# Performance work log

Hardware: AMD Instinct MI355X
Metric: run time of the kernel (lower is better)

Reference implementation:

```python
import jax, jax.numpy as jnp
import numpy as np

D_MODEL = 768
N_HEADS = 12
HEAD = 64
B, T = 2, 2048


def setup_inputs() -> dict:
    key = jax.random.key(0)
    k1, k2, k3 = jax.random.split(key, 3)
    x = jax.random.normal(k1, (B, T, D_MODEL), dtype=jnp.float32)
    W1 = jax.random.normal(k2, (3 * D_MODEL, D_MODEL), dtype=jnp.float32) * (1.0 / np.sqrt(D_MODEL))
    b1 = jnp.zeros((3 * D_MODEL,), dtype=jnp.float32)
    W2 = jax.random.normal(k3, (D_MODEL, D_MODEL), dtype=jnp.float32) * (1.0 / np.sqrt(D_MODEL))
    b2 = jnp.zeros((D_MODEL,), dtype=jnp.float32)
    return {"x": x, "W1": W1, "b1": b1, "W2": W2, "b2": b2}


def reference(x, W1, b1, W2, b2):
    Bx, Tx, C = x.shape
    qkv = jnp.einsum('btc,fc->btf', x, W1) + b1            # (B,T,3C)
    q, k, v = jnp.split(qkv, 3, axis=-1)
    # (B,T,H,Dh) -> (B,H,T,Dh)
    q = q.reshape(Bx, Tx, N_HEADS, HEAD).transpose(0, 2, 1, 3)
    k = k.reshape(Bx, Tx, N_HEADS, HEAD).transpose(0, 2, 1, 3)
    v = v.reshape(Bx, Tx, N_HEADS, HEAD).transpose(0, 2, 1, 3)
    scale = 1.0 / np.sqrt(HEAD)
    scores = jnp.einsum('bhqd,bhkd->bhqk', q, k) * scale   # (B,H,T,T)
    causal = jnp.tril(jnp.ones((Tx, Tx), dtype=bool))
    scores = jnp.where(causal, scores, jnp.finfo(scores.dtype).min)
    attn = jax.nn.softmax(scores, axis=-1)
    o = jnp.einsum('bhqk,bhkd->bhqd', attn, v)             # (B,H,T,Dh)
    o = o.transpose(0, 2, 1, 3).reshape(Bx, Tx, C)
    return jnp.einsum('btc,fc->btf', o, W2) + b2
```

## Files before the change

### kernel.cpp

```cpp
#include <hip/hip_runtime.h>


typedef float f32x4 __attribute__((ext_vector_type(4)));
typedef __bf16 bf16x8 __attribute__((ext_vector_type(8)));
typedef unsigned int u32x4 __attribute__((ext_vector_type(4)));

#define D_MODEL 768
#define F3 2304
#define NHEADS 12
#define HEAD 64
#define BB 2
#define TT 2048
#define MROWS (BB*TT)
#define KDIM 768
#define LOG2E 1.44269504f
#define NX (MROWS*D_MODEL)
#define NW1 (F3*KDIM)
#define NW2 (D_MODEL*KDIM)

__device__ __forceinline__ unsigned short f2bf(float f) {
    unsigned int u = __float_as_uint(f);
    u += 0x7fffu + ((u >> 16) & 1u);
    return (unsigned short)(u >> 16);
}
__device__ __forceinline__ unsigned int pack2bf(float a, float b) {
    unsigned int ua = __float_as_uint(a), ub = __float_as_uint(b);
    ua += 0x7fffu + ((ua >> 16) & 1u);
    ub += 0x7fffu + ((ub >> 16) & 1u);
    return (ua >> 16) | (ub & 0xffff0000u);
}

__device__ __forceinline__ void async_copy16(unsigned short* lds, const unsigned short* g) {
    __builtin_amdgcn_global_load_lds(
        (const __attribute__((address_space(1))) unsigned int*)(const void*)g,
        (__attribute__((address_space(3))) unsigned int*)(void*)lds,
        16, 0, 0);
}

__global__ void prep(const float* __restrict__ x, const float* __restrict__ W1,
                     const float* __restrict__ W2, unsigned short* __restrict__ xb,
                     unsigned short* __restrict__ w1b, unsigned short* __restrict__ w2b) {
    const int i4 = (blockIdx.x * blockDim.x + threadIdx.x) * 4;
    const float* src; unsigned short* dst; int off;
    if (i4 < NX)                  { src = x;  dst = xb;  off = i4; }
    else if (i4 < NX + NW1)       { src = W1; dst = w1b; off = i4 - NX; }
    else if (i4 < NX + NW1 + NW2) { src = W2; dst = w2b; off = i4 - NX - NW1; }
    else return;
    float4 v = *(const float4*)(src + off);
    uint2 o;
    o.x = pack2bf(v.x, v.y);
    o.y = pack2bf(v.z, v.w);
    *(uint2*)(dst + off) = o;
}

__global__ __launch_bounds__(256, 4) void gemm1(
    const unsigned short* __restrict__ A, const unsigned short* __restrict__ Bw,
    const float* __restrict__ bias, int K,
    unsigned short* __restrict__ Qb, unsigned short* __restrict__ Kb,
    unsigned short* __restrict__ VT)
{
    __shared__ unsigned short As[128*64];
    __shared__ unsigned short Bs[96*64];
    const int tid  = threadIdx.x;
    const int wave = tid >> 6;
    const int lane = tid & 63;
    const int quad = lane >> 4;
    const int l16  = lane & 15;

    const int F   = blockIdx.x;
    const int xcd = F & 7;
    const int idx = F >> 3;
    const int bm  = (xcd & 3) * 8 + (idx & 7);
    const int bn  = (xcd >> 2) * 12 + (idx >> 3);
    const int m0  = bm * 128;
    const int n0  = bn * 96;
    const int seg = bn >> 3;

    const int wm = (wave >> 1) * 64;
    const int wn = (wave & 1) * 48;

    f32x4 acc[4][3] = {};

    const unsigned short* Ablk = A + (size_t)m0 * K;
    const unsigned short* Bblk = Bw + (size_t)n0 * K;
    const int srow = tid >> 3;
    const int scol = ((tid & 7) ^ (srow & 7)) * 8;

    for (int k0 = 0; k0 < K; k0 += 64) {
        #pragma unroll
        for (int r = 0; r < 4; ++r)
            async_copy16(As + r*2048 + tid*8,
                         Ablk + (size_t)(r*32 + srow) * K + k0 + scol);
        #pragma unroll
        for (int r = 0; r < 3; ++r)
            async_copy16(Bs + r*2048 + tid*8,
                         Bblk + (size_t)(r*32 + srow) * K + k0 + scol);
        asm volatile("s_waitcnt vmcnt(0)" ::: "memory");
        __syncthreads();

        #pragma unroll
        for (int kc2 = 0; kc2 < 2; ++kc2) {
            const int pos = ((kc2*4 + quad) ^ (l16 & 7)) * 8;
            bf16x8 a[4], b[3];
            #pragma unroll
            for (int i = 0; i < 4; ++i)
                a[i] = *(const bf16x8*)(As + (wm + i*16 + l16)*64 + pos);
            #pragma unroll
            for (int j = 0; j < 3; ++j)
                b[j] = *(const bf16x8*)(Bs + (wn + j*16 + l16)*64 + pos);
            #pragma unroll
            for (int i = 0; i < 4; ++i)
                #pragma unroll
                for (int j = 0; j < 3; ++j)
                    acc[i][j] = __builtin_amdgcn_mfma_f32_16x16x32_bf16(a[i], b[j], acc[i][j], 0, 0, 0);
        }
        __syncthreads();
    }

    if (seg < 2) {
        #pragma unroll
        for (int j = 0; j < 3; ++j) {
            const int n = n0 + wn + j*16 + l16;
            const float bv = bias[n];
            const int f = n - seg * 768;
            const int h = f >> 6, d = f & 63;
            #pragma unroll
            for (int i = 0; i < 4; ++i)
                #pragma unroll
                for (int r = 0; r < 4; ++r) {
                    const int m = m0 + wm + i*16 + quad*4 + r;
                    const int b = m >> 11, t = m & 2047;
                    const size_t idxq = (((size_t)(b*NHEADS + h)) * TT + t) * HEAD + d;
                    const float v = acc[i][j][r] + bv;
                    if (seg == 0) Qb[idxq] = f2bf(v * (0.125f * LOG2E));
                    else          Kb[idxq] = f2bf(v);
                }
        }
    } else {
        #pragma unroll
        for (int j = 0; j < 3; ++j) {
            const int n = n0 + wn + j*16 + l16;
            const float bv = bias[n];
            const int f = n - 1536;
            const int h = f >> 6, d = f & 63;
            #pragma unroll
            for (int i = 0; i < 4; ++i) {
                const int m = m0 + wm + i*16 + quad*4;
                const int b = m >> 11, t = m & 2047;
                uint2 pk;
                pk.x = pack2bf(acc[i][j][0] + bv, acc[i][j][1] + bv);
                pk.y = pack2bf(acc[i][j][2] + bv, acc[i][j][3] + bv);
                *(uint2*)(VT + ((size_t)(b*NHEADS + h) * HEAD + d) * TT + t) = pk;
            }
        }
    }
}

__global__ __launch_bounds__(256, 4) void gemm2(
    const unsigned short* __restrict__ A, const unsigned short* __restrict__ Bw,
    const float* __restrict__ bias, int K, float* __restrict__ Cout)
{
    __shared__ unsigned short As[64*64];
    __shared__ unsigned short Bs[96*64];
    const int tid  = threadIdx.x;
    const int wave = tid >> 6;
    const int lane = tid & 63;
    const int quad = lane >> 4;
    const int l16  = lane & 15;

    const int F   = blockIdx.x;
    const int xcd = F & 7;
    const int idx = F >> 3;
    const int m0  = ((xcd & 3) * 16 + (idx & 15)) * 64;
    const int n0  = ((xcd >> 2) * 4 + (idx >> 4)) * 96;

    const int wm = (wave >> 1) * 32;
    const int wn = (wave & 1) * 48;

    f32x4 acc[2][3] = {};

    const unsigned short* Ablk = A + (size_t)m0 * K;
    const unsigned short* Bblk = Bw + (size_t)n0 * K;
    const int srow = tid >> 3;
    const int scol = ((tid & 7) ^ (srow & 7)) * 8;

    for (int k0 = 0; k0 < K; k0 += 64) {
        #pragma unroll
        for (int r = 0; r < 2; ++r)
            async_copy16(As + r*2048 + tid*8,
                         Ablk + (size_t)(r*32 + srow) * K + k0 + scol);
        #pragma unroll
        for (int r = 0; r < 3; ++r)
            async_copy16(Bs + r*2048 + tid*8,
                         Bblk + (size_t)(r*32 + srow) * K + k0 + scol);
        asm volatile("s_waitcnt vmcnt(0)" ::: "memory");
        __syncthreads();

        #pragma unroll
        for (int kc2 = 0; kc2 < 2; ++kc2) {
            const int pos = ((kc2*4 + quad) ^ (l16 & 7)) * 8;
            bf16x8 a[2], b[3];
            #pragma unroll
            for (int i = 0; i < 2; ++i)
                a[i] = *(const bf16x8*)(As + (wm + i*16 + l16)*64 + pos);
            #pragma unroll
            for (int j = 0; j < 3; ++j)
                b[j] = *(const bf16x8*)(Bs + (wn + j*16 + l16)*64 + pos);
            #pragma unroll
            for (int i = 0; i < 2; ++i)
                #pragma unroll
                for (int j = 0; j < 3; ++j)
                    acc[i][j] = __builtin_amdgcn_mfma_f32_16x16x32_bf16(a[i], b[j], acc[i][j], 0, 0, 0);
        }
        __syncthreads();
    }

    #pragma unroll
    for (int j = 0; j < 3; ++j) {
        const int n = n0 + wn + j*16 + l16;
        const float bv = bias[n];
        #pragma unroll
        for (int i = 0; i < 2; ++i)
            #pragma unroll
            for (int r = 0; r < 4; ++r) {
                const int m = m0 + wm + i*16 + quad*4 + r;
                Cout[(size_t)m * D_MODEL + n] = acc[i][j][r] + bv;
            }
    }
}

__global__ __launch_bounds__(256, 3) void attn(
    const unsigned short* __restrict__ Qb, const unsigned short* __restrict__ Kb,
    const unsigned short* __restrict__ VT, unsigned short* __restrict__ Ob)
{
    __shared__ unsigned short Ks[128*64];
    __shared__ unsigned short Vt[64*128];

    const int tid  = threadIdx.x;
    const int wave = tid >> 6;
    const int lane = tid & 63;
    const int quad = lane >> 4;
    const int l16  = lane & 15;

    const int F    = blockIdx.y * 32 + blockIdx.x;
    const int xcd  = F & 7;
    const int slot = F >> 3;
    const int bh   = xcd * 3 + (slot >> 5);
    const int j    = slot & 31;
    const size_t hbase = (size_t)bh * TT * HEAD;

    const int krow = tid >> 3;
    const int kchunk = ((tid & 7) ^ (krow & 7)) * 8;
    const int vrow = tid >> 4;
    const int vchunk = ((tid & 15) ^ vrow) * 8;

    #pragma unroll 1
    for (int seg = 0; seg < 2; ++seg) {
        const int t   = seg ? (63 - j) : j;
        const int nkt = (t >> 2) + 1;
        const int q0  = t * 32;

        bf16x8 qreg[2][2];
        #pragma unroll
        for (int qs = 0; qs < 2; ++qs) {
            const unsigned short* qp = Qb + hbase + (size_t)(q0 + qs*16 + l16) * HEAD + quad*8;
            qreg[qs][0] = *(const bf16x8*)(qp);
            qreg[qs][1] = *(const bf16x8*)(qp + 32);
        }

        f32x4 oacc[2][4] = {};
        float lst[2] = {0.f, 0.f};

        for (int kt = 0; kt < nkt; ++kt) {
            __syncthreads();

            const unsigned short* ksrc = Kb + hbase + (size_t)kt * 128 * HEAD;
            #pragma unroll
            for (int ii = 0; ii < 4; ++ii)
                async_copy16(Ks + ii*2048 + tid*8,
                             ksrc + (size_t)(ii*32 + krow) * 64 + kchunk);
            #pragma unroll
            for (int ii = 0; ii < 4; ++ii)
                async_copy16(Vt + ii*2048 + tid*8,
                             VT + hbase + (size_t)(ii*16 + vrow) * TT + kt*128 + vchunk);
            asm volatile("s_waitcnt vmcnt(0)" ::: "memory");
            __syncthreads();

            f32x4 s[2][2] = {};
            #pragma unroll
            for (int kc2 = 0; kc2 < 2; ++kc2) {
                const int pos = ((kc2*4 + quad) ^ (l16 & 7)) * 8;
                #pragma unroll
                for (int n = 0; n < 2; ++n) {
                    const bf16x8 ak = *(const bf16x8*)(Ks + (wave*32 + n*16 + l16)*64 + pos);
                    #pragma unroll
                    for (int qs = 0; qs < 2; ++qs)
                        s[n][qs] = __builtin_amdgcn_mfma_f32_16x16x32_bf16(ak, qreg[qs][kc2], s[n][qs], 0, 0, 0);
                }
            }

            if (kt == (t >> 2)) {
                const int kq = kt*128 + wave*32 + quad*4;
                #pragma unroll
                for (int n = 0; n < 2; ++n)
                    #pragma unroll
                    for (int qs = 0; qs < 2; ++qs)
                        #pragma unroll
                        for (int r = 0; r < 4; ++r)
                            if (kq + n*16 + r > q0 + qs*16 + l16) s[n][qs][r] = -1e30f;
            }

            uint2 pck[2][2];
            #pragma unroll
            for (int n = 0; n < 2; ++n)
                #pragma unroll
                for (int qs = 0; qs < 2; ++qs) {
                    const float p0 = exp2f(s[n][qs][0]);
                    const float p1 = exp2f(s[n][qs][1]);
                    const float p2 = exp2f(s[n][qs][2]);
                    const float p3 = exp2f(s[n][qs][3]);
                    lst[qs] += (p0 + p1) + (p2 + p3);
                    pck[n][qs].x = pack2bf(p0, p1);
                    pck[n][qs].y = pack2bf(p2, p3);
                }

            bf16x8 ap[2];
            #pragma unroll
            for (int qs = 0; qs < 2; ++qs) {
                u32x4 pw = {pck[0][qs].x, pck[0][qs].y, pck[1][qs].x, pck[1][qs].y};
                ap[qs] = __builtin_bit_cast(bf16x8, pw);
            }
            const int g1 = wave*4 + (quad >> 1);
            #pragma unroll
            for (int dt = 0; dt < 4; ++dt) {
                const unsigned short* vr = Vt + (dt*16 + l16)*128;
                const int c1 = ((g1     ^ l16) * 8) + (quad & 1) * 4;
                const int c2 = (((g1+2) ^ l16) * 8) + (quad & 1) * 4;
                const uint2 lo = *(const uint2*)(vr + c1);
                const uint2 hi = *(const uint2*)(vr + c2);
                u32x4 vv = {lo.x, lo.y, hi.x, hi.y};
                const bf16x8 bv = __builtin_bit_cast(bf16x8, vv);
                #pragma unroll
                for (int qs = 0; qs < 2; ++qs)
                    oacc[qs][dt] = __builtin_amdgcn_mfma_f32_16x16x32_bf16(ap[qs], bv, oacc[qs][dt], 0, 0, 0);
            }
        }

        #pragma unroll
        for (int qs = 0; qs < 2; ++qs) {
            lst[qs] += __shfl_xor(lst[qs], 16);
            lst[qs] += __shfl_xor(lst[qs], 32);
        }

        __syncthreads();
        {
            float* O1 = (float*)Ks;
            float* O2 = (float*)Ks + 2048;
            float* O3 = (float*)Vt;
            float* Lb = (float*)Vt + 2048;
            if (wave != 0) {
                float* ob = (wave == 1) ? O1 : (wave == 2) ? O2 : O3;
                #pragma unroll
                for (int qs = 0; qs < 2; ++qs)
                    #pragma unroll
                    for (int dt = 0; dt < 4; ++dt)
                        #pragma unroll
                        for (int r = 0; r < 4; ++r)
                            ob[(qs*16 + quad*4 + r)*64 + dt*16 + l16] = oacc[qs][dt][r];
                if (lane < 16) {
                    Lb[(wave-1)*32 + l16]      = lst[0];
                    Lb[(wave-1)*32 + 16 + l16] = lst[1];
                }
            }
            __syncthreads();
            if (wave == 0) {
                float linv[2], lr[2][4];
                #pragma unroll
                for (int qs = 0; qs < 2; ++qs) {
                    const float lt = lst[qs] + Lb[qs*16 + l16] + Lb[32 + qs*16 + l16]
                                             + Lb[64 + qs*16 + l16];
                    linv[qs] = 1.0f / lt;
                }
                #pragma unroll
                for (int qs = 0; qs < 2; ++qs)
                    #pragma unroll
                    for (int r = 0; r < 4; ++r)
                        lr[qs][r] = __shfl(linv[qs], quad*4 + r);
                const int b = bh / NHEADS, h = bh % NHEADS;
                #pragma unroll
                for (int qs = 0; qs < 2; ++qs)
                    #pragma unroll
                    for (int r = 0; r < 4; ++r) {
                        const int m = b * TT + q0 + qs*16 + quad*4 + r;
                        unsigned short* dst = Ob + (size_t)m * D_MODEL + h*HEAD;
                        #pragma unroll
                        for (int dt = 0; dt < 4; ++dt) {
                            const int idx = (qs*16 + quad*4 + r)*64 + dt*16 + l16;
                            const float v = oacc[qs][dt][r] + O1[idx] + O2[idx] + O3[idx];
                            dst[dt*16 + l16] = f2bf(v * lr[qs][r]);
                        }
                    }
            }
        }
    }
}

extern "C" void kernel_launch(void* const* d_in, const int* in_sizes, int n_in,
                              void* d_out, int out_size, void* d_ws, size_t ws_size,
                              hipStream_t stream) {
    const float* x  = (const float*)d_in[0];
    const float* W1 = (const float*)d_in[1];
    const float* b1 = (const float*)d_in[2];
    const float* W2 = (const float*)d_in[3];
    const float* b2 = (const float*)d_in[4];
    float* out = (float*)d_out;

    unsigned short* ws = (unsigned short*)d_ws;
    unsigned short* xb  = ws;
    unsigned short* w1b = xb  + (size_t)NX;
    unsigned short* w2b = w1b + (size_t)NW1;
    unsigned short* Qb  = w2b + (size_t)NW2;
    unsigned short* Kb  = Qb + (size_t)BB*NHEADS*TT*HEAD;
    unsigned short* VT  = Kb + (size_t)BB*NHEADS*TT*HEAD;
    unsigned short* Ob  = VT + (size_t)BB*NHEADS*TT*HEAD;

    prep<<<((NX + NW1 + NW2)/4 + 255)/256, 256, 0, stream>>>(
        x, W1, W2, xb, w1b, w2b);

    gemm1<<<768, 256, 0, stream>>>(
        xb, w1b, b1, KDIM, Qb, Kb, VT);

    attn<<<dim3(32, BB*NHEADS), 256, 0, stream>>>(Qb, Kb, VT, Ob);

    gemm2<<<512, 256, 0, stream>>>(
        Ob, w2b, b2, KDIM, out);
}
```

Baseline: 146.6 us.

## Double-buffer GEMM shared-memory tiles to overlap global loads with MFMA

Both projection GEMMs now split K into 32-wide steps with two LDS buffers, issuing the async copy for the next step before computing the current one. The aim is to hide global-load latency that the old single-buffer load-wait-compute loop exposed. The cost is twice as many barriers and waits per unit of K, plus a new XOR swizzle for the 32-wide rows. Each step also has less MFMA work (one k-chunk instead of two), which may leave too little compute to cover the load.

```diff
diff --git a/kernel.cpp b/kernel.cpp
--- a/kernel.cpp
+++ b/kernel.cpp
@@ -59,8 +59,8 @@
     unsigned short* __restrict__ Qb, unsigned short* __restrict__ Kb,
     unsigned short* __restrict__ VT)
 {
-    __shared__ unsigned short As[128*64];
-    __shared__ unsigned short Bs[96*64];
+    __shared__ unsigned short As[2][128*32];
+    __shared__ unsigned short Bs[2][96*32];
     const int tid  = threadIdx.x;
     const int wave = tid >> 6;
     const int lane = tid & 63;
@@ -83,39 +83,51 @@
 
     const unsigned short* Ablk = A + (size_t)m0 * K;
     const unsigned short* Bblk = Bw + (size_t)n0 * K;
-    const int srow = tid >> 3;
-    const int scol = ((tid & 7) ^ (srow & 7)) * 8;
-
-    for (int k0 = 0; k0 < K; k0 += 64) {
-        #pragma unroll
-        for (int r = 0; r < 4; ++r)
-            async_copy16(As + r*2048 + tid*8,
-                         Ablk + (size_t)(r*32 + srow) * K + k0 + scol);
-        #pragma unroll
-        for (int r = 0; r < 3; ++r)
-            async_copy16(Bs + r*2048 + tid*8,
-                         Bblk + (size_t)(r*32 + srow) * K + k0 + scol);
+
+    const int ra0 = tid >> 2,         ca0 = (tid & 3) ^ ((ra0 >> 1) & 3);
+    const int ra1 = (tid + 256) >> 2, ca1 = (tid & 3) ^ ((ra1 >> 1) & 3);
+    const int rb1 = (tid + 256) >> 2, cb1 = (tid & 3) ^ ((rb1 >> 1) & 3);
+
+    #define G1_STAGE(buf, k0)                                                   \
+        do {                                                                    \
+            async_copy16(&As[buf][tid*8],       Ablk + (size_t)ra0*K + (k0) + ca0*8); \
+            async_copy16(&As[buf][2048 + tid*8],Ablk + (size_t)ra1*K + (k0) + ca1*8); \
+            async_copy16(&Bs[buf][tid*8],       Bblk + (size_t)ra0*K + (k0) + ca0*8); \
+            if (tid < 128)                                                      \
+                async_copy16(&Bs[buf][2048 + tid*8], Bblk + (size_t)rb1*K + (k0) + cb1*8); \
+        } while (0)
+
+    G1_STAGE(0, 0);
+    asm volatile("s_waitcnt vmcnt(0)" ::: "memory");
+    __syncthreads();
+
+    for (int t = 0; t < 24; ++t) {
+        const int cur = t & 1;
+        if (t < 23) G1_STAGE(cur ^ 1, (t + 1) * 32);
+
+        const unsigned short* Ab = As[cur];
+        const unsigned short* Bb = Bs[cur];
+        bf16x8 a[4], b[3];
+        #pragma unroll
+        for (int i = 0; i < 4; ++i) {
+            const int row = wm + i*16 + l16;
+            a[i] = *(const bf16x8*)(Ab + row*32 + ((quad ^ ((row >> 1) & 3)) * 8));
+        }
+        #pragma unroll
+        for (int j = 0; j < 3; ++j) {
+            const int row = wn + j*16 + l16;
+            b[j] = *(const bf16x8*)(Bb + row*32 + ((quad ^ ((row >> 1) & 3)) * 8));
+        }
+        #pragma unroll
+        for (int i = 0; i < 4; ++i)
+            #pragma unroll
+            for (int j = 0; j < 3; ++j)
+                acc[i][j] = __builtin_amdgcn_mfma_f32_16x16x32_bf16(a[i], b[j], acc[i][j], 0, 0, 0);
+
         asm volatile("s_waitcnt vmcnt(0)" ::: "memory");
         __syncthreads();
-
-        #pragma unroll
-        for (int kc2 = 0; kc2 < 2; ++kc2) {
-            const int pos = ((kc2*4 + quad) ^ (l16 & 7)) * 8;
-            bf16x8 a[4], b[3];
-            #pragma unroll
-            for (int i = 0; i < 4; ++i)
-                a[i] = *(const bf16x8*)(As + (wm + i*16 + l16)*64 + pos);
-            #pragma unroll
-            for (int j = 0; j < 3; ++j)
-                b[j] = *(const bf16x8*)(Bs + (wn + j*16 + l16)*64 + pos);
-            #pragma unroll
-            for (int i = 0; i < 4; ++i)
-                #pragma unroll
-                for (int j = 0; j < 3; ++j)
-                    acc[i][j] = __builtin_amdgcn_mfma_f32_16x16x32_bf16(a[i], b[j], acc[i][j], 0, 0, 0);
-        }
-        __syncthreads();
     }
+    #undef G1_STAGE
 
     if (seg < 2) {
         #pragma unroll
@@ -160,8 +172,8 @@
     const unsigned short* __restrict__ A, const unsigned short* __restrict__ Bw,
     const float* __restrict__ bias, int K, float* __restrict__ Cout)
 {
-    __shared__ unsigned short As[64*64];
-    __shared__ unsigned short Bs[96*64];
+    __shared__ unsigned short As[2][64*32];
+    __shared__ unsigned short Bs[2][96*32];
     const int tid  = threadIdx.x;
     const int wave = tid >> 6;
     const int lane = tid & 63;
@@ -181,39 +193,49 @@
 
     const unsigned short* Ablk = A + (size_t)m0 * K;
     const unsigned short* Bblk = Bw + (size_t)n0 * K;
-    const int srow = tid >> 3;
-    const int scol = ((tid & 7) ^ (srow & 7)) * 8;
-
-    for (int k0 = 0; k0 < K; k0 += 64) {
-        #pragma unroll
-        for (int r = 0; r < 2; ++r)
-            async_copy16(As + r*2048 + tid*8,
-                         Ablk + (size_t)(r*32 + srow) * K + k0 + scol);
-        #pragma unroll
-        for (int r = 0; r < 3; ++r)
-            async_copy16(Bs + r*2048 + tid*8,
-                         Bblk + (size_t)(r*32 + srow) * K + k0 + scol);
+
+    const int ra0 = tid >> 2,         ca0 = (tid & 3) ^ ((ra0 >> 1) & 3);
+    const int rb1 = (tid + 256) >> 2, cb1 = (tid & 3) ^ ((rb1 >> 1) & 3);
+
+    #define G2_STAGE(buf, k0)                                                   \
+        do {                                                                    \
+            async_copy16(&As[buf][tid*8],  Ablk + (size_t)ra0*K + (k0) + ca0*8); \
+            async_copy16(&Bs[buf][tid*8],  Bblk + (size_t)ra0*K + (k0) + ca0*8); \
+            if (tid < 128)                                                      \
+                async_copy16(&Bs[buf][2048 + tid*8], Bblk + (size_t)rb1*K + (k0) + cb1*8); \
+        } while (0)
+
+    G2_STAGE(0, 0);
+    asm volatile("s_waitcnt vmcnt(0)" ::: "memory");
+    __syncthreads();
+
+    for (int t = 0; t < 24; ++t) {
+        const int cur = t & 1;
+        if (t < 23) G2_STAGE(cur ^ 1, (t + 1) * 32);
+
+        const unsigned short* Ab = As[cur];
+        const unsigned short* Bb = Bs[cur];
+        bf16x8 a[2], b[3];
+        #pragma unroll
+        for (int i = 0; i < 2; ++i) {
+            const int row = wm + i*16 + l16;
+            a[i] = *(const bf16x8*)(Ab + row*32 + ((quad ^ ((row >> 1) & 3)) * 8));
+        }
+        #pragma unroll
+        for (int j = 0; j < 3; ++j) {
+            const int row = wn + j*16 + l16;
+            b[j] = *(const bf16x8*)(Bb + row*32 + ((quad ^ ((row >> 1) & 3)) * 8));
+        }
+        #pragma unroll
+        for (int i = 0; i < 2; ++i)
+            #pragma unroll
+            for (int j = 0; j < 3; ++j)
+                acc[i][j] = __builtin_amdgcn_mfma_f32_16x16x32_bf16(a[i], b[j], acc[i][j], 0, 0, 0);
+
         asm volatile("s_waitcnt vmcnt(0)" ::: "memory");
         __syncthreads();
-
-        #pragma unroll
-        for (int kc2 = 0; kc2 < 2; ++kc2) {
-            const int pos = ((kc2*4 + quad) ^ (l16 & 7)) * 8;
-            bf16x8 a[2], b[3];
-            #pragma unroll
-            for (int i = 0; i < 2; ++i)
-                a[i] = *(const bf16x8*)(As + (wm + i*16 + l16)*64 + pos);
-            #pragma unroll
-            for (int j = 0; j < 3; ++j)
-                b[j] = *(const bf16x8*)(Bs + (wn + j*16 + l16)*64 + pos);
-            #pragma unroll
-            for (int i = 0; i < 2; ++i)
-                #pragma unroll
-                for (int j = 0; j < 3; ++j)
-                    acc[i][j] = __builtin_amdgcn_mfma_f32_16x16x32_bf16(a[i], b[j], acc[i][j], 0, 0, 0);
-        }
-        __syncthreads();
     }
+    #undef G2_STAGE
 
     #pragma unroll
     for (int j = 0; j < 3; ++j) {
```

After: 150.2 us. +2.5%, slower.

## Share K/V tile loads between paired low and high query blocks in attention

Applied to the files above, without the earlier changes.

Each block used to process its two causal query tiles (j and 63-j) one after the other, loading K/V tiles into shared memory separately for each. The new code runs a single key-tile loop over the longer range and applies each loaded K/V tile to both query tiles, so the shorter tile's K/V loads and LDS fragment reads are no longer repeated. This roughly halves global-to-LDS traffic and synchronisation for the attention stage. The cost is higher register pressure from two sets of Q registers and accumulators, which may lower occupancy.

```diff
diff --git a/kernel.cpp b/kernel.cpp
--- a/kernel.cpp
+++ b/kernel.cpp
@@ -249,160 +249,182 @@
     const int j    = slot & 31;
     const size_t hbase = (size_t)bh * TT * HEAD;
 
+    const int nktl = (j >> 2) + 1;
+    const int nkth = 17 - nktl;
+    const int q0l  = j * 32;
+    const int q0h  = (63 - j) * 32;
+
     const int krow = tid >> 3;
     const int kchunk = ((tid & 7) ^ (krow & 7)) * 8;
     const int vrow = tid >> 4;
     const int vchunk = ((tid & 15) ^ vrow) * 8;
 
-    #pragma unroll 1
-    for (int seg = 0; seg < 2; ++seg) {
-        const int t   = seg ? (63 - j) : j;
-        const int nkt = (t >> 2) + 1;
-        const int q0  = t * 32;
-
-        bf16x8 qreg[2][2];
-        #pragma unroll
-        for (int qs = 0; qs < 2; ++qs) {
-            const unsigned short* qp = Qb + hbase + (size_t)(q0 + qs*16 + l16) * HEAD + quad*8;
-            qreg[qs][0] = *(const bf16x8*)(qp);
-            qreg[qs][1] = *(const bf16x8*)(qp + 32);
-        }
-
-        f32x4 oacc[2][4] = {};
-        float lst[2] = {0.f, 0.f};
-
-        for (int kt = 0; kt < nkt; ++kt) {
-            __syncthreads();
-
-            const unsigned short* ksrc = Kb + hbase + (size_t)kt * 128 * HEAD;
-            #pragma unroll
-            for (int ii = 0; ii < 4; ++ii)
-                async_copy16(Ks + ii*2048 + tid*8,
-                             ksrc + (size_t)(ii*32 + krow) * 64 + kchunk);
-            #pragma unroll
-            for (int ii = 0; ii < 4; ++ii)
-                async_copy16(Vt + ii*2048 + tid*8,
-                             VT + hbase + (size_t)(ii*16 + vrow) * TT + kt*128 + vchunk);
-            asm volatile("s_waitcnt vmcnt(0)" ::: "memory");
-            __syncthreads();
-
-            f32x4 s[2][2] = {};
-            #pragma unroll
-            for (int kc2 = 0; kc2 < 2; ++kc2) {
-                const int pos = ((kc2*4 + quad) ^ (l16 & 7)) * 8;
-                #pragma unroll
-                for (int n = 0; n < 2; ++n) {
-                    const bf16x8 ak = *(const bf16x8*)(Ks + (wave*32 + n*16 + l16)*64 + pos);
-                    #pragma unroll
-                    for (int qs = 0; qs < 2; ++qs)
-                        s[n][qs] = __builtin_amdgcn_mfma_f32_16x16x32_bf16(ak, qreg[qs][kc2], s[n][qs], 0, 0, 0);
-                }
-            }
-
-            if (kt == (t >> 2)) {
-                const int kq = kt*128 + wave*32 + quad*4;
-                #pragma unroll
-                for (int n = 0; n < 2; ++n)
-                    #pragma unroll
-                    for (int qs = 0; qs < 2; ++qs)
-                        #pragma unroll
-                        for (int r = 0; r < 4; ++r)
-                            if (kq + n*16 + r > q0 + qs*16 + l16) s[n][qs][r] = -1e30f;
-            }
-
-            uint2 pck[2][2];
+    bf16x8 qregl[2][2], qregh[2][2];
+    #pragma unroll
+    for (int qs = 0; qs < 2; ++qs) {
+        const unsigned short* ql = Qb + hbase + (size_t)(q0l + qs*16 + l16) * HEAD + quad*8;
+        const unsigned short* qh = Qb + hbase + (size_t)(q0h + qs*16 + l16) * HEAD + quad*8;
+        qregl[qs][0] = *(const bf16x8*)(ql);
+        qregl[qs][1] = *(const bf16x8*)(ql + 32);
+        qregh[qs][0] = *(const bf16x8*)(qh);
+        qregh[qs][1] = *(const bf16x8*)(qh + 32);
+    }
+
+    f32x4 oaccl[2][4] = {}, oacch[2][4] = {};
+    float lstl[2] = {0.f, 0.f}, lsth[2] = {0.f, 0.f};
+
+    const int g1 = wave*4 + (quad >> 1);
+
+    #define TILE_COMPUTE(QREG, OACC, LST, Q0, DOMASK, KT)                       \
+    do {                                                                        \
+        f32x4 s[2][2] = {};                                                     \
+        _Pragma("unroll")                                                       \
+        for (int kc2 = 0; kc2 < 2; ++kc2)                                       \
+            _Pragma("unroll")                                                   \
+            for (int n = 0; n < 2; ++n)                                         \
+                _Pragma("unroll")                                               \
+                for (int qs = 0; qs < 2; ++qs)                                  \
+                    s[n][qs] = __builtin_amdgcn_mfma_f32_16x16x32_bf16(         \
+                        ak[kc2][n], QREG[qs][kc2], s[n][qs], 0, 0, 0);          \
+        if (DOMASK) {                                                           \
+            const int kq = (KT)*128 + wave*32 + quad*4;                         \
+            _Pragma("unroll")                                                   \
+            for (int n = 0; n < 2; ++n)                                         \
+                _Pragma("unroll")                                               \
+                for (int qs = 0; qs < 2; ++qs)                                  \
+                    _Pragma("unroll")                                           \
+                    for (int r = 0; r < 4; ++r)                                 \
+                        if (kq + n*16 + r > (Q0) + qs*16 + l16)                 \
+                            s[n][qs][r] = -1e30f;                               \
+        }                                                                       \
+        uint2 pck[2][2];                                                        \
+        _Pragma("unroll")                                                       \
+        for (int n = 0; n < 2; ++n)                                             \
+            _Pragma("unroll")                                                   \
+            for (int qs = 0; qs < 2; ++qs) {                                    \
+                const float p0 = exp2f(s[n][qs][0]);                            \
+                const float p1 = exp2f(s[n][qs][1]);                            \
+                const float p2 = exp2f(s[n][qs][2]);                            \
+                const float p3 = exp2f(s[n][qs][3]);                            \
+                LST[qs] += (p0 + p1) + (p2 + p3);                               \
+                pck[n][qs].x = pack2bf(p0, p1);                                 \
+                pck[n][qs].y = pack2bf(p2, p3);                                 \
+            }                                                                   \
+        _Pragma("unroll")                                                       \
+        for (int qs = 0; qs < 2; ++qs) {                                        \
+            u32x4 pw = {pck[0][qs].x, pck[0][qs].y, pck[1][qs].x, pck[1][qs].y};\
+            const bf16x8 ap = __builtin_bit_cast(bf16x8, pw);                   \
+            _Pragma("unroll")                                                   \
+            for (int dt = 0; dt < 4; ++dt)                                      \
+                OACC[qs][dt] = __builtin_amdgcn_mfma_f32_16x16x32_bf16(         \
+                    ap, bv[dt], OACC[qs][dt], 0, 0, 0);                         \
+        }                                                                       \
+    } while (0)
+
+    for (int kt = 0; kt < nkth; ++kt) {
+        __syncthreads();
+
+        const unsigned short* ksrc = Kb + hbase + (size_t)kt * 128 * HEAD;
+        #pragma unroll
+        for (int ii = 0; ii < 4; ++ii)
+            async_copy16(Ks + ii*2048 + tid*8,
+                         ksrc + (size_t)(ii*32 + krow) * 64 + kchunk);
+        #pragma unroll
+        for (int ii = 0; ii < 4; ++ii)
+            async_copy16(Vt + ii*2048 + tid*8,
+                         VT + hbase + (size_t)(ii*16 + vrow) * TT + kt*128 + vchunk);
+        asm volatile("s_waitcnt vmcnt(0)" ::: "memory");
+        __syncthreads();
+
+        bf16x8 ak[2][2];
+        #pragma unroll
+        for (int kc2 = 0; kc2 < 2; ++kc2) {
+            const int pos = ((kc2*4 + quad) ^ (l16 & 7)) * 8;
             #pragma unroll
             for (int n = 0; n < 2; ++n)
-                #pragma unroll
-                for (int qs = 0; qs < 2; ++qs) {
-                    const float p0 = exp2f(s[n][qs][0]);
-                    const float p1 = exp2f(s[n][qs][1]);
-                    const float p2 = exp2f(s[n][qs][2]);
-                    const float p3 = exp2f(s[n][qs][3]);
-                    lst[qs] += (p0 + p1) + (p2 + p3);
-                    pck[n][qs].x = pack2bf(p0, p1);
-                    pck[n][qs].y = pack2bf(p2, p3);
-                }
-
-            bf16x8 ap[2];
-            #pragma unroll
-            for (int qs = 0; qs < 2; ++qs) {
-                u32x4 pw = {pck[0][qs].x, pck[0][qs].y, pck[1][qs].x, pck[1][qs].y};
-                ap[qs] = __builtin_bit_cast(bf16x8, pw);
-            }
-            const int g1 = wave*4 + (quad >> 1);
-            #pragma unroll
-            for (int dt = 0; dt < 4; ++dt) {
-                const unsigned short* vr = Vt + (dt*16 + l16)*128;
-                const int c1 = ((g1     ^ l16) * 8) + (quad & 1) * 4;
-                const int c2 = (((g1+2) ^ l16) * 8) + (quad & 1) * 4;
-                const uint2 lo = *(const uint2*)(vr + c1);
-                const uint2 hi = *(const uint2*)(vr + c2);
-                u32x4 vv = {lo.x, lo.y, hi.x, hi.y};
-                const bf16x8 bv = __builtin_bit_cast(bf16x8, vv);
-                #pragma unroll
-                for (int qs = 0; qs < 2; ++qs)
-                    oacc[qs][dt] = __builtin_amdgcn_mfma_f32_16x16x32_bf16(ap[qs], bv, oacc[qs][dt], 0, 0, 0);
-            }
-        }
-
-        #pragma unroll
-        for (int qs = 0; qs < 2; ++qs) {
-            lst[qs] += __shfl_xor(lst[qs], 16);
-            lst[qs] += __shfl_xor(lst[qs], 32);
-        }
-
-        __syncthreads();
-        {
-            float* O1 = (float*)Ks;
-            float* O2 = (float*)Ks + 2048;
-            float* O3 = (float*)Vt;
-            float* Lb = (float*)Vt + 2048;
-            if (wave != 0) {
-                float* ob = (wave == 1) ? O1 : (wave == 2) ? O2 : O3;
-                #pragma unroll
-                for (int qs = 0; qs < 2; ++qs)
-                    #pragma unroll
-                    for (int dt = 0; dt < 4; ++dt)
-                        #pragma unroll
-                        for (int r = 0; r < 4; ++r)
-                            ob[(qs*16 + quad*4 + r)*64 + dt*16 + l16] = oacc[qs][dt][r];
-                if (lane < 16) {
-                    Lb[(wave-1)*32 + l16]      = lst[0];
-                    Lb[(wave-1)*32 + 16 + l16] = lst[1];
-                }
-            }
-            __syncthreads();
-            if (wave == 0) {
-                float linv[2], lr[2][4];
-                #pragma unroll
-                for (int qs = 0; qs < 2; ++qs) {
-                    const float lt = lst[qs] + Lb[qs*16 + l16] + Lb[32 + qs*16 + l16]
-                                             + Lb[64 + qs*16 + l16];
-                    linv[qs] = 1.0f / lt;
-                }
-                #pragma unroll
-                for (int qs = 0; qs < 2; ++qs)
-                    #pragma unroll
-                    for (int r = 0; r < 4; ++r)
-                        lr[qs][r] = __shfl(linv[qs], quad*4 + r);
-                const int b = bh / NHEADS, h = bh % NHEADS;
-                #pragma unroll
-                for (int qs = 0; qs < 2; ++qs)
-                    #pragma unroll
-                    for (int r = 0; r < 4; ++r) {
-                        const int m = b * TT + q0 + qs*16 + quad*4 + r;
-                        unsigned short* dst = Ob + (size_t)m * D_MODEL + h*HEAD;
-                        #pragma unroll
-                        for (int dt = 0; dt < 4; ++dt) {
-                            const int idx = (qs*16 + quad*4 + r)*64 + dt*16 + l16;
-                            const float v = oacc[qs][dt][r] + O1[idx] + O2[idx] + O3[idx];
-                            dst[dt*16 + l16] = f2bf(v * lr[qs][r]);
-                        }
-                    }
-            }
-        }
-    }
+                ak[kc2][n] = *(const bf16x8*)(Ks + (wave*32 + n*16 + l16)*64 + pos);
+        }
+        bf16x8 bv[4];
+        #pragma unroll
+        for (int dt = 0; dt < 4; ++dt) {
+            const unsigned short* vr = Vt + (dt*16 + l16)*128;
+            const int c1 = ((g1     ^ l16) * 8) + (quad & 1) * 4;
+            const int c2 = (((g1+2) ^ l16) * 8) + (quad & 1) * 4;
+            const uint2 lo = *(const uint2*)(vr + c1);
+            const uint2 hi = *(const uint2*)(vr + c2);
+            u32x4 vv = {lo.x, lo.y, hi.x, hi.y};
+            bv[dt] = __builtin_bit_cast(bf16x8, vv);
+        }
+
+        TILE_COMPUTE(qregh, oacch, lsth, q0h, (kt == nkth - 1), kt);
+        if (kt < nktl)
+            TILE_COMPUTE(qregl, oaccl, lstl, q0l, (kt == nktl - 1), kt);
+    }
+    #undef TILE_COMPUTE
+
+    #pragma unroll
+    for (int qs = 0; qs < 2; ++qs) {
+        lstl[qs] += __shfl_xor(lstl[qs], 16);
+        lstl[qs] += __shfl_xor(lstl[qs], 32);
+        lsth[qs] += __shfl_xor(lsth[qs], 16);
+        lsth[qs] += __shfl_xor(lsth[qs], 32);
+    }
+
+    #define COMBINE(OACC, LST, Q0)                                              \
+    do {                                                                        \
+        float* O1 = (float*)Ks;                                                 \
+        float* O2 = (float*)Ks + 2048;                                          \
+        float* O3 = (float*)Vt;                                                 \
+        float* Lb = (float*)Vt + 2048;                                          \
+        __syncthreads();                                                        \
+        if (wave != 0) {                                                        \
+            float* ob = (wave == 1) ? O1 : (wave == 2) ? O2 : O3;               \
+            _Pragma("unroll")                                                   \
+            for (int qs = 0; qs < 2; ++qs)                                      \
+                _Pragma("unroll")                                               \
+                for (int dt = 0; dt < 4; ++dt)                                  \
+                    _Pragma("unroll")                                           \
+                    for (int r = 0; r < 4; ++r)                                 \
+                        ob[(qs*16 + quad*4 + r)*64 + dt*16 + l16] = OACC[qs][dt][r]; \
+            if (lane < 16) {                                                    \
+                Lb[(wave-1)*32 + l16]      = LST[0];                            \
+                Lb[(wave-1)*32 + 16 + l16] = LST[1];                            \
+            }                                                                   \
+        }                                                                       \
+        __syncthreads();                                                        \
+        if (wave == 0) {                                                        \
+            float linv[2], lr[2][4];                                            \
+            _Pragma("unroll")                                                   \
+            for (int qs = 0; qs < 2; ++qs) {                                    \
+                const float lt = LST[qs] + Lb[qs*16 + l16] + Lb[32 + qs*16 + l16] \
+                                         + Lb[64 + qs*16 + l16];                \
+                linv[qs] = 1.0f / lt;                                           \
+            }                                                                   \
+            _Pragma("unroll")                                                   \
+            for (int qs = 0; qs < 2; ++qs)                                      \
+                _Pragma("unroll")                                               \
+                for (int r = 0; r < 4; ++r)                                     \
+                    lr[qs][r] = __shfl(linv[qs], quad*4 + r);                   \
+            const int b = bh / NHEADS, h = bh % NHEADS;                         \
+            _Pragma("unroll")                                                   \
+            for (int qs = 0; qs < 2; ++qs)                                      \
+                _Pragma("unroll")                                               \
+                for (int r = 0; r < 4; ++r) {                                   \
+                    const int m = b * TT + (Q0) + qs*16 + quad*4 + r;           \
+                    unsigned short* dst = Ob + (size_t)m * D_MODEL + h*HEAD;    \
+                    _Pragma("unroll")                                           \
+                    for (int dt = 0; dt < 4; ++dt) {                            \
+                        const int idx = (qs*16 + quad*4 + r)*64 + dt*16 + l16;  \
+                        const float v = OACC[qs][dt][r] + O1[idx] + O2[idx] + O3[idx]; \
+                        dst[dt*16 + l16] = f2bf(v * lr[qs][r]);                 \
+                    }                                                           \
+                }                                                               \
+        }                                                                       \
+    } while (0)
+
+    COMBINE(oaccl, lstl, q0l);
+    COMBINE(oacch, lsth, q0h);
+    #undef COMBINE
 }
 
 extern "C" void kernel_launch(void* const* d_in, const int* in_sizes, int n_in,
```

Measured after the change: 152.3 us. 3.9% more time.

## Split attention block across 8 waves by query half and key slice

Applied to the files above, without the earlier changes.

The attention kernel now launches 512 threads per block instead of 256. Each wave handles one 16-row query half and one 32-key slice of the 128-key tile, instead of both query halves. Per-wave accumulators and MFMA work are halved, and each thread issues half as many async loads per tile. The cross-wave reduction is rearranged into six partial buffers in shared memory. The aim is more waves to hide latency and fewer registers per wave, at the cost of more barrier participants and a different occupancy target.

```diff
diff --git a/kernel.cpp b/kernel.cpp
--- a/kernel.cpp
+++ b/kernel.cpp
@@ -229,7 +229,7 @@
     }
 }
 
-__global__ __launch_bounds__(256, 3) void attn(
+__global__ __launch_bounds__(512, 6) void attn(
     const unsigned short* __restrict__ Qb, const unsigned short* __restrict__ Kb,
     const unsigned short* __restrict__ VT, unsigned short* __restrict__ Ob)
 {
@@ -241,6 +241,8 @@
     const int lane = tid & 63;
     const int quad = lane >> 4;
     const int l16  = lane & 15;
+    const int qh   = wave & 1;
+    const int ks   = wave >> 1;
 
     const int F    = blockIdx.y * 32 + blockIdx.x;
     const int xcd  = F & 7;
@@ -249,88 +251,78 @@
     const int j    = slot & 31;
     const size_t hbase = (size_t)bh * TT * HEAD;
 
-    const int krow = tid >> 3;
-    const int kchunk = ((tid & 7) ^ (krow & 7)) * 8;
-    const int vrow = tid >> 4;
-    const int vchunk = ((tid & 15) ^ vrow) * 8;
+    const int k0r = tid >> 3;
+    const int k0c = ((tid & 7) ^ (k0r & 7)) * 8;
+    const int k1r = k0r + 64;
+    const int k1c = ((tid & 7) ^ (k1r & 7)) * 8;
+    const int v0r = tid >> 4;
+    const int v1r = v0r + 32;
+    const int vc  = ((tid & 15) ^ (v0r & 15)) * 8;
 
     #pragma unroll 1
     for (int seg = 0; seg < 2; ++seg) {
         const int t   = seg ? (63 - j) : j;
         const int nkt = (t >> 2) + 1;
         const int q0  = t * 32;
-
-        bf16x8 qreg[2][2];
-        #pragma unroll
-        for (int qs = 0; qs < 2; ++qs) {
-            const unsigned short* qp = Qb + hbase + (size_t)(q0 + qs*16 + l16) * HEAD + quad*8;
-            qreg[qs][0] = *(const bf16x8*)(qp);
-            qreg[qs][1] = *(const bf16x8*)(qp + 32);
-        }
-
-        f32x4 oacc[2][4] = {};
-        float lst[2] = {0.f, 0.f};
+        const int qg  = q0 + qh*16 + l16;
+
+        bf16x8 qreg[2];
+        {
+            const unsigned short* qp = Qb + hbase + (size_t)qg * HEAD + quad*8;
+            qreg[0] = *(const bf16x8*)(qp);
+            qreg[1] = *(const bf16x8*)(qp + 32);
+        }
+
+        f32x4 oacc[4] = {};
+        float lst = 0.f;
 
         for (int kt = 0; kt < nkt; ++kt) {
             __syncthreads();
 
             const unsigned short* ksrc = Kb + hbase + (size_t)kt * 128 * HEAD;
-            #pragma unroll
-            for (int ii = 0; ii < 4; ++ii)
-                async_copy16(Ks + ii*2048 + tid*8,
-                             ksrc + (size_t)(ii*32 + krow) * 64 + kchunk);
-            #pragma unroll
-            for (int ii = 0; ii < 4; ++ii)
-                async_copy16(Vt + ii*2048 + tid*8,
-                             VT + hbase + (size_t)(ii*16 + vrow) * TT + kt*128 + vchunk);
+            async_copy16(Ks + tid*8,        ksrc + (size_t)k0r * 64 + k0c);
+            async_copy16(Ks + 4096 + tid*8, ksrc + (size_t)k1r * 64 + k1c);
+            const unsigned short* vsrc = VT + hbase + kt*128;
+            async_copy16(Vt + tid*8,        vsrc + (size_t)v0r * TT + vc);
+            async_copy16(Vt + 4096 + tid*8, vsrc + (size_t)v1r * TT + vc);
             asm volatile("s_waitcnt vmcnt(0)" ::: "memory");
             __syncthreads();
 
-            f32x4 s[2][2] = {};
+            f32x4 s[2] = {};
             #pragma unroll
             for (int kc2 = 0; kc2 < 2; ++kc2) {
                 const int pos = ((kc2*4 + quad) ^ (l16 & 7)) * 8;
                 #pragma unroll
                 for (int n = 0; n < 2; ++n) {
-                    const bf16x8 ak = *(const bf16x8*)(Ks + (wave*32 + n*16 + l16)*64 + pos);
-                    #pragma unroll
-                    for (int qs = 0; qs < 2; ++qs)
-                        s[n][qs] = __builtin_amdgcn_mfma_f32_16x16x32_bf16(ak, qreg[qs][kc2], s[n][qs], 0, 0, 0);
+                    const bf16x8 ak = *(const bf16x8*)(Ks + (ks*32 + n*16 + l16)*64 + pos);
+                    s[n] = __builtin_amdgcn_mfma_f32_16x16x32_bf16(ak, qreg[kc2], s[n], 0, 0, 0);
                 }
             }
 
             if (kt == (t >> 2)) {
-                const int kq = kt*128 + wave*32 + quad*4;
+                const int kq = kt*128 + ks*32 + quad*4;
                 #pragma unroll
                 for (int n = 0; n < 2; ++n)
                     #pragma unroll
-                    for (int qs = 0; qs < 2; ++qs)
-                        #pragma unroll
-                        for (int r = 0; r < 4; ++r)
-                            if (kq + n*16 + r > q0 + qs*16 + l16) s[n][qs][r] = -1e30f;
-            }
-
-            uint2 pck[2][2];
-            #pragma unroll
-            for (int n = 0; n < 2; ++n)
-                #pragma unroll
-                for (int qs = 0; qs < 2; ++qs) {
-                    const float p0 = exp2f(s[n][qs][0]);
-                    const float p1 = exp2f(s[n][qs][1]);
-                    const float p2 = exp2f(s[n][qs][2]);
-                    const float p3 = exp2f(s[n][qs][3]);
-                    lst[qs] += (p0 + p1) + (p2 + p3);
-                    pck[n][qs].x = pack2bf(p0, p1);
-                    pck[n][qs].y = pack2bf(p2, p3);
-                }
-
-            bf16x8 ap[2];
-            #pragma unroll
-            for (int qs = 0; qs < 2; ++qs) {
-                u32x4 pw = {pck[0][qs].x, pck[0][qs].y, pck[1][qs].x, pck[1][qs].y};
-                ap[qs] = __builtin_bit_cast(bf16x8, pw);
-            }
-            const int g1 = wave*4 + (quad >> 1);
+                    for (int r = 0; r < 4; ++r)
+                        if (kq + n*16 + r > qg) s[n][r] = -1e30f;
+            }
+
+            uint2 pck[2];
+            #pragma unroll
+            for (int n = 0; n < 2; ++n) {
+                const float p0 = exp2f(s[n][0]);
+                const float p1 = exp2f(s[n][1]);
+                const float p2 = exp2f(s[n][2]);
+                const float p3 = exp2f(s[n][3]);
+                lst += (p0 + p1) + (p2 + p3);
+                pck[n].x = pack2bf(p0, p1);
+                pck[n].y = pack2bf(p2, p3);
+            }
+
+            u32x4 pw = {pck[0].x, pck[0].y, pck[1].x, pck[1].y};
+            const bf16x8 ap = __builtin_bit_cast(bf16x8, pw);
+            const int g1 = ks*4 + (quad >> 1);
             #pragma unroll
             for (int dt = 0; dt < 4; ++dt) {
                 const unsigned short* vr = Vt + (dt*16 + l16)*128;
@@ -340,66 +332,53 @@
                 const uint2 hi = *(const uint2*)(vr + c2);
                 u32x4 vv = {lo.x, lo.y, hi.x, hi.y};
                 const bf16x8 bv = __builtin_bit_cast(bf16x8, vv);
-                #pragma unroll
-                for (int qs = 0; qs < 2; ++qs)
-                    oacc[qs][dt] = __builtin_amdgcn_mfma_f32_16x16x32_bf16(ap[qs], bv, oacc[qs][dt], 0, 0, 0);
-            }
-        }
-
-        #pragma unroll
-        for (int qs = 0; qs < 2; ++qs) {
-            lst[qs] += __shfl_xor(lst[qs], 16);
-            lst[qs] += __shfl_xor(lst[qs], 32);
-        }
+                oacc[dt] = __builtin_amdgcn_mfma_f32_16x16x32_bf16(ap, bv, oacc[dt], 0, 0, 0);
+            }
+        }
+
+        lst += __shfl_xor(lst, 16);
+        lst += __shfl_xor(lst, 32);
 
         __syncthreads();
         {
-            float* O1 = (float*)Ks;
-            float* O2 = (float*)Ks + 2048;
-            float* O3 = (float*)Vt;
-            float* Lb = (float*)Vt + 2048;
-            if (wave != 0) {
-                float* ob = (wave == 1) ? O1 : (wave == 2) ? O2 : O3;
-                #pragma unroll
-                for (int qs = 0; qs < 2; ++qs)
-                    #pragma unroll
-                    for (int dt = 0; dt < 4; ++dt)
-                        #pragma unroll
-                        for (int r = 0; r < 4; ++r)
-                            ob[(qs*16 + quad*4 + r)*64 + dt*16 + l16] = oacc[qs][dt][r];
-                if (lane < 16) {
-                    Lb[(wave-1)*32 + l16]      = lst[0];
-                    Lb[(wave-1)*32 + 16 + l16] = lst[1];
-                }
-            }
-            __syncthreads();
-            if (wave == 0) {
-                float linv[2], lr[2][4];
-                #pragma unroll
-                for (int qs = 0; qs < 2; ++qs) {
-                    const float lt = lst[qs] + Lb[qs*16 + l16] + Lb[32 + qs*16 + l16]
-                                             + Lb[64 + qs*16 + l16];
-                    linv[qs] = 1.0f / lt;
-                }
-                #pragma unroll
-                for (int qs = 0; qs < 2; ++qs)
+            float* KsF = (float*)Ks;
+            float* VtF = (float*)Vt;
+            if (ks != 0) {
+                const int b = qh*3 + (ks - 1);
+                float* ob = (b < 4) ? (KsF + b*1024) : (VtF + (b - 4)*1024);
+                #pragma unroll
+                for (int dt = 0; dt < 4; ++dt)
                     #pragma unroll
                     for (int r = 0; r < 4; ++r)
-                        lr[qs][r] = __shfl(linv[qs], quad*4 + r);
+                        ob[(quad*4 + r)*64 + dt*16 + l16] = oacc[dt][r];
+                if (lane < 16)
+                    VtF[2048 + b*16 + l16] = lst;
+            }
+            __syncthreads();
+            if (ks == 0) {
+                const int b0 = qh*3;
+                const float* o1 = (b0     < 4) ? (KsF + b0*1024)     : (VtF + (b0 - 4)*1024);
+                const float* o2 = (b0 + 1 < 4) ? (KsF + (b0+1)*1024) : (VtF + (b0 - 3)*1024);
+                const float* o3 = (b0 + 2 < 4) ? (KsF + (b0+2)*1024) : (VtF + (b0 - 2)*1024);
+                const float lt = lst + VtF[2048 + b0*16 + l16]
+                                     + VtF[2048 + (b0+1)*16 + l16]
+                                     + VtF[2048 + (b0+2)*16 + l16];
+                const float linv = 1.0f / lt;
+                float lr[4];
+                #pragma unroll
+                for (int r = 0; r < 4; ++r) lr[r] = __shfl(linv, quad*4 + r);
                 const int b = bh / NHEADS, h = bh % NHEADS;
                 #pragma unroll
-                for (int qs = 0; qs < 2; ++qs)
+                for (int r = 0; r < 4; ++r) {
+                    const int m = b*TT + q0 + qh*16 + quad*4 + r;
+                    unsigned short* dst = Ob + (size_t)m * D_MODEL + h*HEAD;
                     #pragma unroll
-                    for (int r = 0; r < 4; ++r) {
-                        const int m = b * TT + q0 + qs*16 + quad*4 + r;
-                        unsigned short* dst = Ob + (size_t)m * D_MODEL + h*HEAD;
-                        #pragma unroll
-                        for (int dt = 0; dt < 4; ++dt) {
-                            const int idx = (qs*16 + quad*4 + r)*64 + dt*16 + l16;
-                            const float v = oacc[qs][dt][r] + O1[idx] + O2[idx] + O3[idx];
-                            dst[dt*16 + l16] = f2bf(v * lr[qs][r]);
-                        }
+                    for (int dt = 0; dt < 4; ++dt) {
+                        const int idx = (quad*4 + r)*64 + dt*16 + l16;
+                        const float v = oacc[dt][r] + o1[idx] + o2[idx] + o3[idx];
+                        dst[dt*16 + l16] = f2bf(v * lr[r]);
                     }
+                }
             }
         }
     }
@@ -430,7 +409,7 @@
     gemm1<<<768, 256, 0, stream>>>(
         xb, w1b, b1, KDIM, Qb, Kb, VT);
 
-    attn<<<dim3(32, BB*NHEADS), 256, 0, stream>>>(Qb, Kb, VT, Ob);
+    attn<<<dim3(32, BB*NHEADS), 512, 0, stream>>>(Qb, Kb, VT, Ob);
 
     gemm2<<<512, 256, 0, stream>>>(
         Ob, w2b, b2, KDIM, out);
```

Result: slower. 153.8 us (+4.9%).
